# Performance work log

Hardware: AMD Instinct MI355X
Metric: run time of the kernel (lower is better)

## Reference

```python
import jax, jax.numpy as jnp
import numpy as np

B, S, D = 8, 2048, 512

def setup_inputs() -> dict:
    key = jax.random.key(0)
    ks = jax.random.split(key, 9)
    scale = 1.0 / np.sqrt(D)
    return {
        "x": jax.random.normal(ks[0], (B, S, D), dtype=jnp.float32),
        "attention_mask": jax.random.uniform(ks[1], (B, S), dtype=jnp.float32),
        "Wq": jax.random.normal(ks[2], (D, D), dtype=jnp.float32) * scale,
        "bq": jax.random.normal(ks[3], (D,), dtype=jnp.float32) * 0.01,
        "Wk": jax.random.normal(ks[4], (D, D), dtype=jnp.float32) * scale,
        "bk": jax.random.normal(ks[5], (D,), dtype=jnp.float32) * 0.01,
        "Wv": jax.random.normal(ks[6], (D, D), dtype=jnp.float32) * scale,
        "bv": jax.random.normal(ks[7], (D,), dtype=jnp.float32) * 0.01,
    }

def reference(x, attention_mask, Wq, bq, Wk, bk, Wv, bv):
    # Single-head self-attention, full O(S^2) scores as in the original.
    q = jnp.einsum('bsd,df->bsf', x, Wq) + bq  # [B,S,D]
    k = jnp.einsum('bsd,df->bsf', x, Wk) + bk
    v = jnp.einsum('bsd,df->bsf', x, Wv) + bv
    scores = jnp.einsum('bqd,bkd->bqk', q, k) / jnp.sqrt(jnp.float32(D))  # [B,S,S]
    attn = jax.nn.softmax(scores, axis=2)
    weighted = jnp.einsum('bqk,bkd->bqd', attn, v)  # [B,S,D]
    # mask applied multiplicatively to the output, per original code
    return weighted * attention_mask[:, :, None]
```

## Files before the change

### kernel.cpp

```cpp
#include <hip/hip_runtime.h>
#include <math.h>
#include <stdint.h>


typedef _Float16 f16x8 __attribute__((ext_vector_type(8)));
typedef _Float16 f16x4 __attribute__((ext_vector_type(4)));
typedef _Float16 f16x2 __attribute__((ext_vector_type(2)));
typedef float f32x4 __attribute__((ext_vector_type(4)));

__device__ __forceinline__ void async16(const _Float16* g, _Float16* l) {
    __builtin_amdgcn_global_load_lds(
        (const __attribute__((address_space(1))) unsigned int*)(uintptr_t)g,
        (__attribute__((address_space(3))) unsigned int*)(unsigned int)(uintptr_t)l,
        16, 0, 0);
}

__device__ __forceinline__ float frag_sum8(f16x8 v, float acc) {
#if __has_builtin(__builtin_amdgcn_fdot2)
    const f16x2 one2 = {(_Float16)1.f, (_Float16)1.f};
    const f16x2* p = (const f16x2*)&v;
    acc = __builtin_amdgcn_fdot2(p[0], one2, acc, false);
    acc = __builtin_amdgcn_fdot2(p[1], one2, acc, false);
    acc = __builtin_amdgcn_fdot2(p[2], one2, acc, false);
    acc = __builtin_amdgcn_fdot2(p[3], one2, acc, false);
#else
#pragma unroll
    for (int j = 0; j < 8; j++) acc += (float)v[j];
#endif
    return acc;
}

#define MFMA16(a, b, c) __builtin_amdgcn_mfma_f32_16x16x32_f16(a, b, c, 0, 0, 0)
#define BAR() __builtin_amdgcn_s_barrier()
#define LGKM0() asm volatile("s_waitcnt lgkmcnt(0)" ::: "memory")

template <int NT, bool WITH_RS>
__device__ __forceinline__ void core128sq(
    const _Float16* __restrict__ A, const _Float16* __restrict__ B,
    int ld, int row0, int col0, _Float16* sm, f32x4 acc[4][4], float rs[4])
{
    const int tid = threadIdx.x, lane = tid & 63, wave = tid >> 6;
    const int wm = wave >> 1, wn = wave & 1;
    const int rc = lane >> 3;
    const int swz = ((lane & 7) ^ rc) * 8;
    const int fr = lane & 15, q = lane >> 4, fx = fr & 7;
    const size_t laneoff = (size_t)rc * ld + swz;

    const _Float16* gA[4]; int lA[4];
#pragma unroll
    for (int i = 0; i < 4; i++) {
        int c = wave * 4 + i;
        gA[i] = A + (size_t)(row0 + 8 * c) * ld + laneoff;
        lA[i] = c * 512;
    }
    const _Float16* gBe[2]; const _Float16* gBl[2]; int lBe[2], lBl[2];
#pragma unroll
    for (int i = 0; i < 2; i++) {
        int idx = wave * 2 + i;
        int je = (idx & 3) + (idx >> 2) * 8;
        int jl = je + 4;
        gBe[i] = B + (size_t)(col0 + 8 * je) * ld + laneoff;
        gBl[i] = B + (size_t)(col0 + 8 * jl) * ld + laneoff;
        lBe[i] = 8192 + je * 512;
        lBl[i] = 8192 + jl * 512;
    }

#pragma unroll
    for (int i = 0; i < 4; i++) async16(gA[i], sm + lA[i]);
#pragma unroll
    for (int i = 0; i < 2; i++) async16(gBe[i], sm + lBe[i]);
#pragma unroll
    for (int i = 0; i < 2; i++) async16(gBl[i], sm + lBl[i]);
#pragma unroll
    for (int i = 0; i < 4; i++) async16(gA[i] + 64, sm + 16384 + lA[i]);
#pragma unroll
    for (int i = 0; i < 2; i++) async16(gBe[i] + 64, sm + 16384 + lBe[i]);
    asm volatile("s_waitcnt vmcnt(6)" ::: "memory");
    BAR();

#pragma unroll 2
    for (int t = 0; t < NT; ++t) {
        const _Float16* As = sm + (t & 1) * 16384;
        const _Float16* Bs = As + 8192;
        f16x8 af[4][2], b0f[2][2], b1f[2][2];

#pragma unroll
        for (int m = 0; m < 4; m++)
#pragma unroll
            for (int s = 0; s < 2; s++) {
                int ra = wm * 64 + m * 16 + fr;
                af[m][s] = *(const f16x8*)&As[ra * 64 + (((s * 4 + q) ^ fx) * 8)];
            }
#pragma unroll
        for (int n = 0; n < 2; n++)
#pragma unroll
            for (int s = 0; s < 2; s++) {
                int rb = wn * 64 + n * 16 + fr;
                b0f[n][s] = *(const f16x8*)&Bs[rb * 64 + (((s * 4 + q) ^ fx) * 8)];
            }
        if (t + 1 < NT) {
            _Float16* nb = sm + ((t + 1) & 1) * 16384;
#pragma unroll
            for (int i = 0; i < 2; i++)
                async16(gBl[i] + (t + 1) * 64, nb + lBl[i]);
        }
        BAR(); LGKM0();
        if (WITH_RS) {
#pragma unroll
            for (int m = 0; m < 4; m++)
#pragma unroll
                for (int s = 0; s < 2; s++) rs[m] = frag_sum8(af[m][s], rs[m]);
        }
        __builtin_amdgcn_s_setprio(1);
#pragma unroll
        for (int s = 0; s < 2; s++)
#pragma unroll
            for (int m = 0; m < 4; m++)
#pragma unroll
                for (int n = 0; n < 2; n++)
                    acc[m][n] = MFMA16(af[m][s], b0f[n][s], acc[m][n]);
        __builtin_amdgcn_s_setprio(0);
        BAR();

#pragma unroll
        for (int n = 0; n < 2; n++)
#pragma unroll
            for (int s = 0; s < 2; s++) {
                int rb = wn * 64 + (2 + n) * 16 + fr;
                b1f[n][s] = *(const f16x8*)&Bs[rb * 64 + (((s * 4 + q) ^ fx) * 8)];
            }
        if (t + 2 < NT) {
            _Float16* stg = sm + (t & 1) * 16384;
            const int k2 = (t + 2) * 64;
#pragma unroll
            for (int i = 0; i < 4; i++) async16(gA[i] + k2, stg + lA[i]);
#pragma unroll
            for (int i = 0; i < 2; i++) async16(gBe[i] + k2, stg + lBe[i]);
            asm volatile("s_waitcnt vmcnt(6)" ::: "memory");
        } else {
            asm volatile("s_waitcnt vmcnt(0)" ::: "memory");
        }
        BAR(); LGKM0();
        __builtin_amdgcn_s_setprio(1);
#pragma unroll
        for (int s = 0; s < 2; s++)
#pragma unroll
            for (int m = 0; m < 4; m++)
#pragma unroll
                for (int n = 0; n < 2; n++)
                    acc[m][2 + n] = MFMA16(af[m][s], b1f[n][s], acc[m][2 + n]);
        __builtin_amdgcn_s_setprio(0);
        BAR();
    }
}

__global__ __launch_bounds__(256) void prep(
    const float* __restrict__ x,
    const float* __restrict__ Wq, const float* __restrict__ Wk,
    const float* __restrict__ Wv,
    _Float16* __restrict__ Xh,
    _Float16* __restrict__ WqT, _Float16* __restrict__ WkT,
    _Float16* __restrict__ WvT)
{
    const int bid = blockIdx.x;
    if (bid < 8192) {
        int i = (bid * 256 + threadIdx.x) * 4;
        float4 v = *(const float4*)(x + i);
        f16x4 h;
        h.x = (_Float16)v.x; h.y = (_Float16)v.y;
        h.z = (_Float16)v.z; h.w = (_Float16)v.w;
        *(f16x4*)&Xh[i] = h;
    } else {
        int t = bid - 8192;
        int z = t >> 10;
        const float* W = (z == 0) ? Wq : (z == 1) ? Wk : Wv;
        _Float16* Wt   = (z == 0) ? WqT : (z == 1) ? WkT : WvT;
        int idx = (t & 1023) * 256 + threadIdx.x;
        int n = idx >> 9, k = idx & 511;
        Wt[idx] = (_Float16)W[k * 512 + n];
    }
}

__global__ __launch_bounds__(256, 2) void proj_mfma(
    const _Float16* __restrict__ Xh,
    const _Float16* __restrict__ WqT, const float* __restrict__ bq,
    const _Float16* __restrict__ WkT, const float* __restrict__ bk,
    const _Float16* __restrict__ WvT, const float* __restrict__ bv,
    _Float16* __restrict__ Qh, _Float16* __restrict__ Kh,
    _Float16* __restrict__ Vt)
{
    __shared__ __align__(16) _Float16 smem[2 * 16384];
    const int z = blockIdx.z;
    f32x4 acc[4][4];
#pragma unroll
    for (int i = 0; i < 4; i++)
#pragma unroll
        for (int j = 0; j < 4; j++) acc[i][j] = (f32x4){0.f, 0.f, 0.f, 0.f};
    float rs_unused[4];

    const int lane = threadIdx.x & 63, wave = threadIdx.x >> 6;
    const int wm = wave >> 1, wn = wave & 1;
    const int er = (lane >> 4) * 4, ec = lane & 15;

    if (z < 2) {
        const _Float16* Wt = (z == 0) ? WqT : WkT;
        const float* bias  = (z == 0) ? bq : bk;
        _Float16* P        = (z == 0) ? Qh : Kh;
        const float sc     = (z == 0) ? 0.04419417382415922f : 1.0f;
        const int row0 = blockIdx.x * 128, col0 = blockIdx.y * 128;
        core128sq<8, false>(Xh, Wt, 512, row0, col0, smem, acc, rs_unused);
#pragma unroll
        for (int tm = 0; tm < 4; tm++)
#pragma unroll
            for (int tn = 0; tn < 4; tn++) {
                int col = col0 + wn * 64 + tn * 16 + ec;
                float bb = bias[col];
#pragma unroll
                for (int r = 0; r < 4; r++) {
                    int row = row0 + wm * 64 + tm * 16 + er + r;
                    P[(size_t)row * 512 + col] = (_Float16)((acc[tm][tn][r] + bb) * sc);
                }
            }
    } else {
        const int row0 = blockIdx.y * 128;
        const int col0 = blockIdx.x * 128;
        core128sq<8, false>(WvT, Xh, 512, row0, col0, smem, acc, rs_unused);
#pragma unroll
        for (int tm = 0; tm < 4; tm++)
#pragma unroll
            for (int tn = 0; tn < 4; tn++) {
                int col = col0 + wn * 64 + tn * 16 + ec;
                size_t obase = (size_t)(col >> 11) * (512 * 2048) + (col & 2047);
#pragma unroll
                for (int r = 0; r < 4; r++) {
                    int row = row0 + wm * 64 + tm * 16 + er + r;
                    Vt[obase + (size_t)row * 2048] = (_Float16)(acc[tm][tn][r] + bv[row]);
                }
            }
    }
}

__global__ __launch_bounds__(256, 2) void scores_mfma(
    const _Float16* __restrict__ Qh, const _Float16* __restrict__ Kh,
    _Float16* __restrict__ Sh)
{
    __shared__ __align__(16) _Float16 smem[2 * 16384];
    const int bid = blockIdx.x;
    const int b   = bid & 7;
    const int rem = bid >> 3;
    const int col0 = (rem & 15) * 128;
    const int row0 = (rem >> 4) * 128;

    const _Float16* A = Qh + (size_t)b * 2048 * 512;
    const _Float16* B = Kh + (size_t)b * 2048 * 512;
    _Float16* S = Sh + (size_t)b * 2048 * 2048;

    f32x4 acc[4][4];
#pragma unroll
    for (int i = 0; i < 4; i++)
#pragma unroll
        for (int j = 0; j < 4; j++) acc[i][j] = (f32x4){0.f, 0.f, 0.f, 0.f};
    float rs_unused[4];

    core128sq<8, false>(A, B, 512, row0, col0, smem, acc, rs_unused);

    const int lane = threadIdx.x & 63, wave = threadIdx.x >> 6;
    const int wm = wave >> 1, wn = wave & 1;
    const int er = (lane >> 4) * 4, ec = lane & 15;
#pragma unroll
    for (int tm = 0; tm < 4; tm++)
#pragma unroll
        for (int tn = 0; tn < 4; tn++) {
            int col = col0 + wn * 64 + tn * 16 + ec;
#pragma unroll
            for (int r = 0; r < 4; r++) {
                int row = row0 + wm * 64 + tm * 16 + er + r;
                S[(size_t)row * 2048 + col] = (_Float16)__expf(acc[tm][tn][r]);
            }
        }
}

__global__ __launch_bounds__(256, 2) void av_mfma(
    const _Float16* __restrict__ Sh, const _Float16* __restrict__ Vt,
    const float* __restrict__ mask, float* __restrict__ out)
{
    __shared__ __align__(16) _Float16 smem[2 * 16384];
    const int bid = blockIdx.x;
    const int b   = bid & 7;
    const int rem = bid >> 3;
    const int col0 = (rem & 3) * 128;
    const int row0 = (rem >> 2) * 128;

    const _Float16* A = Sh + (size_t)b * 2048 * 2048;
    const _Float16* B = Vt + (size_t)b * 512 * 2048;
    float* O = out + (size_t)b * 2048 * 512;
    const float* mk = mask + (size_t)b * 2048;

    f32x4 acc[4][4];
#pragma unroll
    for (int i = 0; i < 4; i++)
#pragma unroll
        for (int j = 0; j < 4; j++) acc[i][j] = (f32x4){0.f, 0.f, 0.f, 0.f};
    float rs[4] = {0.f, 0.f, 0.f, 0.f};

    core128sq<32, true>(A, B, 2048, row0, col0, smem, acc, rs);

    const int lane = threadIdx.x & 63, wave = threadIdx.x >> 6;
    const int wm = wave >> 1, wn = wave & 1;
    const int er = (lane >> 4) * 4, ec = lane & 15;

#pragma unroll
    for (int tm = 0; tm < 4; tm++) {
        rs[tm] += __shfl_xor(rs[tm], 16, 64);
        rs[tm] += __shfl_xor(rs[tm], 32, 64);
    }
    __syncthreads();
    float* l_s = (float*)smem;
    if (wn == 0 && lane < 16) {
#pragma unroll
        for (int tm = 0; tm < 4; tm++) l_s[wm * 64 + tm * 16 + lane] = rs[tm];
    }
    __syncthreads();

#pragma unroll
    for (int tm = 0; tm < 4; tm++)
#pragma unroll
        for (int r = 0; r < 4; r++) {
            int lrow = wm * 64 + tm * 16 + er + r;
            int row = row0 + lrow;
            float s = mk[row] / l_s[lrow];
#pragma unroll
            for (int tn = 0; tn < 4; tn++) {
                int col = col0 + wn * 64 + tn * 16 + ec;
                O[(size_t)row * 512 + col] = acc[tm][tn][r] * s;
            }
        }
}

extern "C" void kernel_launch(void* const* d_in, const int* in_sizes, int n_in,
                              void* d_out, int out_size, void* d_ws, size_t ws_size,
                              hipStream_t stream) {
    const float* x    = (const float*)d_in[0];
    const float* mask = (const float*)d_in[1];
    const float* Wq   = (const float*)d_in[2];
    const float* bq   = (const float*)d_in[3];
    const float* Wk   = (const float*)d_in[4];
    const float* bk   = (const float*)d_in[5];
    const float* Wv   = (const float*)d_in[6];
    const float* bv   = (const float*)d_in[7];
    float* out = (float*)d_out;

    const size_t BSD = (size_t)8 * 2048 * 512;
    _Float16* base = (_Float16*)d_ws;
    _Float16* Qh  = base;
    _Float16* Kh  = Qh + BSD;
    _Float16* Vt  = Kh + BSD;
    _Float16* WqT = Vt + BSD;
    _Float16* WkT = WqT + 512 * 512;
    _Float16* WvT = WkT + 512 * 512;
    _Float16* Xh  = WvT + 512 * 512;
    _Float16* Sh  = Xh;

    prep<<<dim3(8192 + 3 * 1024), dim3(256), 0, stream>>>(
        x, Wq, Wk, Wv, Xh, WqT, WkT, WvT);
    proj_mfma<<<dim3(128, 4, 3), dim3(256), 0, stream>>>(
        Xh, WqT, bq, WkT, bk, WvT, bv, Qh, Kh, Vt);
    scores_mfma<<<dim3(2048), dim3(256), 0, stream>>>(Qh, Kh, Sh);
    av_mfma<<<dim3(512), dim3(256), 0, stream>>>(Sh, Vt, mask, out);
}
```

Measured before the change: 210.9 us.

## Fuse all four stages into one cooperative persistent kernel with grid syncs

Replaces the four separate launches (prep, projection, scores, AV) with a single cooperative kernel of 512 blocks. It loops over work units per stage and separates stages with grid.sync(). The aim is to remove per-launch overhead and the idle tails between kernels. In exchange, each stage is capped at 512 resident blocks, grid-wide barriers are added, and the old multi-kernel path is kept as a fallback if the cooperative launch fails.

```diff
diff --git a/kernel.cpp b/kernel.cpp
--- a/kernel.cpp
+++ b/kernel.cpp
@@ -1,6 +1,9 @@
 #include <hip/hip_runtime.h>
+#include <hip/hip_cooperative_groups.h>
 #include <math.h>
 #include <stdint.h>
+
+namespace cg = cooperative_groups;
 
 
 typedef _Float16 f16x8 __attribute__((ext_vector_type(8)));
@@ -154,43 +157,39 @@
     }
 }
 
-__global__ __launch_bounds__(256) void prep(
-    const float* __restrict__ x,
+__device__ __forceinline__ void prep_unit(
+    int u, const float* __restrict__ x,
     const float* __restrict__ Wq, const float* __restrict__ Wk,
     const float* __restrict__ Wv,
-    _Float16* __restrict__ Xh,
-    _Float16* __restrict__ WqT, _Float16* __restrict__ WkT,
-    _Float16* __restrict__ WvT)
-{
-    const int bid = blockIdx.x;
-    if (bid < 8192) {
-        int i = (bid * 256 + threadIdx.x) * 4;
+    _Float16* Xh, _Float16* WqT, _Float16* WkT, _Float16* WvT)
+{
+    const int tid = threadIdx.x;
+    if (u < 8192) {
+        int i = (u * 256 + tid) * 4;
         float4 v = *(const float4*)(x + i);
         f16x4 h;
         h.x = (_Float16)v.x; h.y = (_Float16)v.y;
         h.z = (_Float16)v.z; h.w = (_Float16)v.w;
         *(f16x4*)&Xh[i] = h;
     } else {
-        int t = bid - 8192;
+        int t = u - 8192;
         int z = t >> 10;
         const float* W = (z == 0) ? Wq : (z == 1) ? Wk : Wv;
         _Float16* Wt   = (z == 0) ? WqT : (z == 1) ? WkT : WvT;
-        int idx = (t & 1023) * 256 + threadIdx.x;
+        int idx = (t & 1023) * 256 + tid;
         int n = idx >> 9, k = idx & 511;
         Wt[idx] = (_Float16)W[k * 512 + n];
     }
 }
 
-__global__ __launch_bounds__(256, 2) void proj_mfma(
-    const _Float16* __restrict__ Xh,
-    const _Float16* __restrict__ WqT, const float* __restrict__ bq,
-    const _Float16* __restrict__ WkT, const float* __restrict__ bk,
-    const _Float16* __restrict__ WvT, const float* __restrict__ bv,
-    _Float16* __restrict__ Qh, _Float16* __restrict__ Kh,
-    _Float16* __restrict__ Vt)
-{
-    __shared__ __align__(16) _Float16 smem[2 * 16384];
-    const int z = blockIdx.z;
+__device__ __forceinline__ void proj_unit(
+    int u, const _Float16* Xh,
+    const _Float16* WqT, const float* __restrict__ bq,
+    const _Float16* WkT, const float* __restrict__ bk,
+    const _Float16* WvT, const float* __restrict__ bv,
+    _Float16* Qh, _Float16* Kh, _Float16* Vt, _Float16* smem)
+{
+    const int bx = u & 127, by = (u >> 7) & 3, z = u >> 9;
     f32x4 acc[4][4];
 #pragma unroll
     for (int i = 0; i < 4; i++)
@@ -207,7 +206,7 @@
         const float* bias  = (z == 0) ? bq : bk;
         _Float16* P        = (z == 0) ? Qh : Kh;
         const float sc     = (z == 0) ? 0.04419417382415922f : 1.0f;
-        const int row0 = blockIdx.x * 128, col0 = blockIdx.y * 128;
+        const int row0 = bx * 128, col0 = by * 128;
         core128sq<8, false>(Xh, Wt, 512, row0, col0, smem, acc, rs_unused);
 #pragma unroll
         for (int tm = 0; tm < 4; tm++)
@@ -222,8 +221,8 @@
                 }
             }
     } else {
-        const int row0 = blockIdx.y * 128;
-        const int col0 = blockIdx.x * 128;
+        const int row0 = by * 128;
+        const int col0 = bx * 128;
         core128sq<8, false>(WvT, Xh, 512, row0, col0, smem, acc, rs_unused);
 #pragma unroll
         for (int tm = 0; tm < 4; tm++)
@@ -240,14 +239,12 @@
     }
 }
 
-__global__ __launch_bounds__(256, 2) void scores_mfma(
-    const _Float16* __restrict__ Qh, const _Float16* __restrict__ Kh,
-    _Float16* __restrict__ Sh)
-{
-    __shared__ __align__(16) _Float16 smem[2 * 16384];
-    const int bid = blockIdx.x;
-    const int b   = bid & 7;
-    const int rem = bid >> 3;
+__device__ __forceinline__ void scores_unit(
+    int u, const _Float16* Qh, const _Float16* Kh, _Float16* Sh,
+    _Float16* smem)
+{
+    const int b   = u & 7;
+    const int rem = u >> 3;
     const int col0 = (rem & 15) * 128;
     const int row0 = (rem >> 4) * 128;
 
@@ -280,14 +277,12 @@
         }
 }
 
-__global__ __launch_bounds__(256, 2) void av_mfma(
-    const _Float16* __restrict__ Sh, const _Float16* __restrict__ Vt,
-    const float* __restrict__ mask, float* __restrict__ out)
-{
-    __shared__ __align__(16) _Float16 smem[2 * 16384];
-    const int bid = blockIdx.x;
-    const int b   = bid & 7;
-    const int rem = bid >> 3;
+__device__ __forceinline__ void av_unit(
+    int u, const _Float16* Sh, const _Float16* Vt,
+    const float* __restrict__ mask, float* __restrict__ out, _Float16* smem)
+{
+    const int b   = u & 7;
+    const int rem = u >> 3;
     const int col0 = (rem & 3) * 128;
     const int row0 = (rem >> 2) * 128;
 
@@ -335,6 +330,67 @@
                 O[(size_t)row * 512 + col] = acc[tm][tn][r] * s;
             }
         }
+}
+
+__global__ __launch_bounds__(256, 2) void fused_all(
+    const float* __restrict__ x, const float* __restrict__ mask,
+    const float* __restrict__ Wq, const float* __restrict__ bq,
+    const float* __restrict__ Wk, const float* __restrict__ bk,
+    const float* __restrict__ Wv, const float* __restrict__ bv,
+    float* __restrict__ out,
+    _Float16* Qh, _Float16* Kh, _Float16* Vt,
+    _Float16* WqT, _Float16* WkT, _Float16* WvT,
+    _Float16* Xh, _Float16* Sh)
+{
+    __shared__ __align__(16) _Float16 smem[2 * 16384];
+    cg::grid_group grid = cg::this_grid();
+    const int bid = blockIdx.x;
+
+    for (int u = bid; u < 11264; u += 512)
+        prep_unit(u, x, Wq, Wk, Wv, Xh, WqT, WkT, WvT);
+    grid.sync();
+    for (int u = bid; u < 1536; u += 512)
+        proj_unit(u, Xh, WqT, bq, WkT, bk, WvT, bv, Qh, Kh, Vt, smem);
+    grid.sync();
+    for (int u = bid; u < 2048; u += 512)
+        scores_unit(u, Qh, Kh, Sh, smem);
+    grid.sync();
+    av_unit(bid, Sh, Vt, mask, out, smem);
+}
+
+__global__ __launch_bounds__(256) void prep_k(
+    const float* __restrict__ x,
+    const float* __restrict__ Wq, const float* __restrict__ Wk,
+    const float* __restrict__ Wv,
+    _Float16* Xh, _Float16* WqT, _Float16* WkT, _Float16* WvT)
+{
+    prep_unit(blockIdx.x, x, Wq, Wk, Wv, Xh, WqT, WkT, WvT);
+}
+
+__global__ __launch_bounds__(256, 2) void proj_k(
+    const _Float16* Xh,
+    const _Float16* WqT, const float* __restrict__ bq,
+    const _Float16* WkT, const float* __restrict__ bk,
+    const _Float16* WvT, const float* __restrict__ bv,
+    _Float16* Qh, _Float16* Kh, _Float16* Vt)
+{
+    __shared__ __align__(16) _Float16 smem[2 * 16384];
+    proj_unit(blockIdx.x, Xh, WqT, bq, WkT, bk, WvT, bv, Qh, Kh, Vt, smem);
+}
+
+__global__ __launch_bounds__(256, 2) void scores_k(
+    const _Float16* Qh, const _Float16* Kh, _Float16* Sh)
+{
+    __shared__ __align__(16) _Float16 smem[2 * 16384];
+    scores_unit(blockIdx.x, Qh, Kh, Sh, smem);
+}
+
+__global__ __launch_bounds__(256, 2) void av_k(
+    const _Float16* Sh, const _Float16* Vt,
+    const float* __restrict__ mask, float* __restrict__ out)
+{
+    __shared__ __align__(16) _Float16 smem[2 * 16384];
+    av_unit(blockIdx.x, Sh, Vt, mask, out, smem);
 }
 
 extern "C" void kernel_launch(void* const* d_in, const int* in_sizes, int n_in,
@@ -361,10 +417,19 @@
     _Float16* Xh  = WvT + 512 * 512;
     _Float16* Sh  = Xh;
 
-    prep<<<dim3(8192 + 3 * 1024), dim3(256), 0, stream>>>(
-        x, Wq, Wk, Wv, Xh, WqT, WkT, WvT);
-    proj_mfma<<<dim3(128, 4, 3), dim3(256), 0, stream>>>(
-        Xh, WqT, bq, WkT, bk, WvT, bv, Qh, Kh, Vt);
-    scores_mfma<<<dim3(2048), dim3(256), 0, stream>>>(Qh, Kh, Sh);
-    av_mfma<<<dim3(512), dim3(256), 0, stream>>>(Sh, Vt, mask, out);
-}
+    void* kargs[] = {
+        (void*)&x, (void*)&mask, (void*)&Wq, (void*)&bq, (void*)&Wk,
+        (void*)&bk, (void*)&Wv, (void*)&bv, (void*)&out,
+        (void*)&Qh, (void*)&Kh, (void*)&Vt,
+        (void*)&WqT, (void*)&WkT, (void*)&WvT, (void*)&Xh, (void*)&Sh };
+    hipError_t err = hipLaunchCooperativeKernel(
+        (const void*)fused_all, dim3(512), dim3(256), kargs, 0, stream);
+    if (err != hipSuccess) {
+        prep_k<<<dim3(8192 + 3 * 1024), dim3(256), 0, stream>>>(
+            x, Wq, Wk, Wv, Xh, WqT, WkT, WvT);
+        proj_k<<<dim3(1536), dim3(256), 0, stream>>>(
+            Xh, WqT, bq, WkT, bk, WvT, bv, Qh, Kh, Vt);
+        scores_k<<<dim3(2048), dim3(256), 0, stream>>>(Qh, Kh, Sh);
+        av_k<<<dim3(512), dim3(256), 0, stream>>>(Sh, Vt, mask, out);
+    }
+}
```

After: 436.9 us. 107% more time.

## Split each 128x128 MFMA tile across eight waves instead of four

Applied to the files above, without the earlier changes.

The shared GEMM core now runs with 512 threads, so each wave computes a 64x32 sub-tile instead of 64x64. The double-buffered async-to-LDS pipeline is rebuilt so the two A row-halves are staged in separate phases instead of the two B halves, and the av row-sum accumulation is split the same way. All three MFMA kernels use the new core with launch bounds of 512 threads and 4 blocks. The aim is more resident waves per CU to hide load latency, at the cost of more B-fragment LDS reads per FLOP, more barrier traffic, and a tighter per-thread register budget that could cause spills.

```diff
diff --git a/kernel.cpp b/kernel.cpp
--- a/kernel.cpp
+++ b/kernel.cpp
@@ -35,57 +35,45 @@
 #define LGKM0() asm volatile("s_waitcnt lgkmcnt(0)" ::: "memory")
 
 template <int NT, bool WITH_RS>
-__device__ __forceinline__ void core128sq(
+__device__ __forceinline__ void core8w(
     const _Float16* __restrict__ A, const _Float16* __restrict__ B,
-    int ld, int row0, int col0, _Float16* sm, f32x4 acc[4][4], float rs[4])
+    int ld, int row0, int col0, _Float16* sm, f32x4 acc[4][2], float rs[4])
 {
     const int tid = threadIdx.x, lane = tid & 63, wave = tid >> 6;
-    const int wm = wave >> 1, wn = wave & 1;
+    const int wm = wave >> 2, wn = wave & 3;
     const int rc = lane >> 3;
     const int swz = ((lane & 7) ^ rc) * 8;
     const int fr = lane & 15, q = lane >> 4, fx = fr & 7;
     const size_t laneoff = (size_t)rc * ld + swz;
 
-    const _Float16* gA[4]; int lA[4];
-#pragma unroll
-    for (int i = 0; i < 4; i++) {
-        int c = wave * 4 + i;
-        gA[i] = A + (size_t)(row0 + 8 * c) * ld + laneoff;
-        lA[i] = c * 512;
-    }
-    const _Float16* gBe[2]; const _Float16* gBl[2]; int lBe[2], lBl[2];
-#pragma unroll
-    for (int i = 0; i < 2; i++) {
-        int idx = wave * 2 + i;
-        int je = (idx & 3) + (idx >> 2) * 8;
-        int jl = je + 4;
-        gBe[i] = B + (size_t)(col0 + 8 * je) * ld + laneoff;
-        gBl[i] = B + (size_t)(col0 + 8 * jl) * ld + laneoff;
-        lBe[i] = 8192 + je * 512;
-        lBl[i] = 8192 + jl * 512;
-    }
-
-#pragma unroll
-    for (int i = 0; i < 4; i++) async16(gA[i], sm + lA[i]);
-#pragma unroll
-    for (int i = 0; i < 2; i++) async16(gBe[i], sm + lBe[i]);
-#pragma unroll
-    for (int i = 0; i < 2; i++) async16(gBl[i], sm + lBl[i]);
-#pragma unroll
-    for (int i = 0; i < 4; i++) async16(gA[i] + 64, sm + 16384 + lA[i]);
-#pragma unroll
-    for (int i = 0; i < 2; i++) async16(gBe[i] + 64, sm + 16384 + lBe[i]);
-    asm volatile("s_waitcnt vmcnt(6)" ::: "memory");
+    const int ah0c = (wave & 3) + (wave >> 2) * 8;
+    const int ah1c = ah0c + 4;
+    const int b0c = 2 * wave, b1c = b0c + 1;
+    const _Float16* gAh0 = A + (size_t)(row0 + 8 * ah0c) * ld + laneoff;
+    const _Float16* gAh1 = A + (size_t)(row0 + 8 * ah1c) * ld + laneoff;
+    const _Float16* gB0  = B + (size_t)(col0 + 8 * b0c) * ld + laneoff;
+    const _Float16* gB1  = B + (size_t)(col0 + 8 * b1c) * ld + laneoff;
+    const int lAh0 = ah0c * 512, lAh1 = ah1c * 512;
+    const int lB0 = 8192 + b0c * 512, lB1 = 8192 + b1c * 512;
+
+    async16(gAh0, sm + lAh0);
+    async16(gAh1, sm + lAh1);
+    async16(gB0,  sm + lB0);
+    async16(gB1,  sm + lB1);
+    async16(gB0 + 64,  sm + 16384 + lB0);
+    async16(gB1 + 64,  sm + 16384 + lB1);
+    async16(gAh0 + 64, sm + 16384 + lAh0);
+    asm volatile("s_waitcnt vmcnt(3)" ::: "memory");
     BAR();
 
 #pragma unroll 2
     for (int t = 0; t < NT; ++t) {
         const _Float16* As = sm + (t & 1) * 16384;
         const _Float16* Bs = As + 8192;
-        f16x8 af[4][2], b0f[2][2], b1f[2][2];
-
-#pragma unroll
-        for (int m = 0; m < 4; m++)
+        f16x8 af[2][2], bf[2][2];
+
+#pragma unroll
+        for (int m = 0; m < 2; m++)
 #pragma unroll
             for (int s = 0; s < 2; s++) {
                 int ra = wm * 64 + m * 16 + fr;
@@ -95,19 +83,15 @@
         for (int n = 0; n < 2; n++)
 #pragma unroll
             for (int s = 0; s < 2; s++) {
-                int rb = wn * 64 + n * 16 + fr;
-                b0f[n][s] = *(const f16x8*)&Bs[rb * 64 + (((s * 4 + q) ^ fx) * 8)];
-            }
-        if (t + 1 < NT) {
-            _Float16* nb = sm + ((t + 1) & 1) * 16384;
-#pragma unroll
-            for (int i = 0; i < 2; i++)
-                async16(gBl[i] + (t + 1) * 64, nb + lBl[i]);
-        }
+                int rb = wn * 32 + n * 16 + fr;
+                bf[n][s] = *(const f16x8*)&Bs[rb * 64 + (((s * 4 + q) ^ fx) * 8)];
+            }
+        if (t + 1 < NT)
+            async16(gAh1 + (t + 1) * 64, sm + ((t + 1) & 1) * 16384 + lAh1);
         BAR(); LGKM0();
         if (WITH_RS) {
 #pragma unroll
-            for (int m = 0; m < 4; m++)
+            for (int m = 0; m < 2; m++)
 #pragma unroll
                 for (int s = 0; s < 2; s++) rs[m] = frag_sum8(af[m][s], rs[m]);
         }
@@ -115,41 +99,48 @@
 #pragma unroll
         for (int s = 0; s < 2; s++)
 #pragma unroll
-            for (int m = 0; m < 4; m++)
+            for (int m = 0; m < 2; m++)
 #pragma unroll
                 for (int n = 0; n < 2; n++)
-                    acc[m][n] = MFMA16(af[m][s], b0f[n][s], acc[m][n]);
+                    acc[m][n] = MFMA16(af[m][s], bf[n][s], acc[m][n]);
         __builtin_amdgcn_s_setprio(0);
         BAR();
 
 #pragma unroll
-        for (int n = 0; n < 2; n++)
+        for (int m = 0; m < 2; m++)
 #pragma unroll
             for (int s = 0; s < 2; s++) {
-                int rb = wn * 64 + (2 + n) * 16 + fr;
-                b1f[n][s] = *(const f16x8*)&Bs[rb * 64 + (((s * 4 + q) ^ fx) * 8)];
+                int ra = wm * 64 + (2 + m) * 16 + fr;
+                af[m][s] = *(const f16x8*)&As[ra * 64 + (((s * 4 + q) ^ fx) * 8)];
             }
         if (t + 2 < NT) {
             _Float16* stg = sm + (t & 1) * 16384;
             const int k2 = (t + 2) * 64;
-#pragma unroll
-            for (int i = 0; i < 4; i++) async16(gA[i] + k2, stg + lA[i]);
-#pragma unroll
-            for (int i = 0; i < 2; i++) async16(gBe[i] + k2, stg + lBe[i]);
-            asm volatile("s_waitcnt vmcnt(6)" ::: "memory");
+            async16(gB0 + k2,  stg + lB0);
+            async16(gB1 + k2,  stg + lB1);
+            async16(gAh0 + k2, stg + lAh0);
+        }
+        BAR(); LGKM0();
+        if (WITH_RS) {
+#pragma unroll
+            for (int m = 0; m < 2; m++)
+#pragma unroll
+                for (int s = 0; s < 2; s++) rs[2 + m] = frag_sum8(af[m][s], rs[2 + m]);
+        }
+        __builtin_amdgcn_s_setprio(1);
+#pragma unroll
+        for (int s = 0; s < 2; s++)
+#pragma unroll
+            for (int m = 0; m < 2; m++)
+#pragma unroll
+                for (int n = 0; n < 2; n++)
+                    acc[2 + m][n] = MFMA16(af[m][s], bf[n][s], acc[2 + m][n]);
+        __builtin_amdgcn_s_setprio(0);
+        if (t + 2 < NT) {
+            asm volatile("s_waitcnt vmcnt(3)" ::: "memory");
         } else {
             asm volatile("s_waitcnt vmcnt(0)" ::: "memory");
         }
-        BAR(); LGKM0();
-        __builtin_amdgcn_s_setprio(1);
-#pragma unroll
-        for (int s = 0; s < 2; s++)
-#pragma unroll
-            for (int m = 0; m < 4; m++)
-#pragma unroll
-                for (int n = 0; n < 2; n++)
-                    acc[m][2 + n] = MFMA16(af[m][s], b1f[n][s], acc[m][2 + n]);
-        __builtin_amdgcn_s_setprio(0);
         BAR();
     }
 }
@@ -181,7 +172,7 @@
     }
 }
 
-__global__ __launch_bounds__(256, 2) void proj_mfma(
+__global__ __launch_bounds__(512, 4) void proj_mfma(
     const _Float16* __restrict__ Xh,
     const _Float16* __restrict__ WqT, const float* __restrict__ bq,
     const _Float16* __restrict__ WkT, const float* __restrict__ bk,
@@ -191,15 +182,15 @@
 {
     __shared__ __align__(16) _Float16 smem[2 * 16384];
     const int z = blockIdx.z;
-    f32x4 acc[4][4];
+    f32x4 acc[4][2];
 #pragma unroll
     for (int i = 0; i < 4; i++)
 #pragma unroll
-        for (int j = 0; j < 4; j++) acc[i][j] = (f32x4){0.f, 0.f, 0.f, 0.f};
+        for (int j = 0; j < 2; j++) acc[i][j] = (f32x4){0.f, 0.f, 0.f, 0.f};
     float rs_unused[4];
 
     const int lane = threadIdx.x & 63, wave = threadIdx.x >> 6;
-    const int wm = wave >> 1, wn = wave & 1;
+    const int wm = wave >> 2, wn = wave & 3;
     const int er = (lane >> 4) * 4, ec = lane & 15;
 
     if (z < 2) {
@@ -208,12 +199,12 @@
         _Float16* P        = (z == 0) ? Qh : Kh;
         const float sc     = (z == 0) ? 0.04419417382415922f : 1.0f;
         const int row0 = blockIdx.x * 128, col0 = blockIdx.y * 128;
-        core128sq<8, false>(Xh, Wt, 512, row0, col0, smem, acc, rs_unused);
+        core8w<8, false>(Xh, Wt, 512, row0, col0, smem, acc, rs_unused);
 #pragma unroll
         for (int tm = 0; tm < 4; tm++)
 #pragma unroll
-            for (int tn = 0; tn < 4; tn++) {
-                int col = col0 + wn * 64 + tn * 16 + ec;
+            for (int tn = 0; tn < 2; tn++) {
+                int col = col0 + wn * 32 + tn * 16 + ec;
                 float bb = bias[col];
 #pragma unroll
                 for (int r = 0; r < 4; r++) {
@@ -224,12 +215,12 @@
     } else {
         const int row0 = blockIdx.y * 128;
         const int col0 = blockIdx.x * 128;
-        core128sq<8, false>(WvT, Xh, 512, row0, col0, smem, acc, rs_unused);
+        core8w<8, false>(WvT, Xh, 512, row0, col0, smem, acc, rs_unused);
 #pragma unroll
         for (int tm = 0; tm < 4; tm++)
 #pragma unroll
-            for (int tn = 0; tn < 4; tn++) {
-                int col = col0 + wn * 64 + tn * 16 + ec;
+            for (int tn = 0; tn < 2; tn++) {
+                int col = col0 + wn * 32 + tn * 16 + ec;
                 size_t obase = (size_t)(col >> 11) * (512 * 2048) + (col & 2047);
 #pragma unroll
                 for (int r = 0; r < 4; r++) {
@@ -240,7 +231,7 @@
     }
 }
 
-__global__ __launch_bounds__(256, 2) void scores_mfma(
+__global__ __launch_bounds__(512, 4) void scores_mfma(
     const _Float16* __restrict__ Qh, const _Float16* __restrict__ Kh,
     _Float16* __restrict__ Sh)
 {
@@ -255,23 +246,23 @@
     const _Float16* B = Kh + (size_t)b * 2048 * 512;
     _Float16* S = Sh + (size_t)b * 2048 * 2048;
 
-    f32x4 acc[4][4];
+    f32x4 acc[4][2];
 #pragma unroll
     for (int i = 0; i < 4; i++)
 #pragma unroll
-        for (int j = 0; j < 4; j++) acc[i][j] = (f32x4){0.f, 0.f, 0.f, 0.f};
+        for (int j = 0; j < 2; j++) acc[i][j] = (f32x4){0.f, 0.f, 0.f, 0.f};
     float rs_unused[4];
 
-    core128sq<8, false>(A, B, 512, row0, col0, smem, acc, rs_unused);
+    core8w<8, false>(A, B, 512, row0, col0, smem, acc, rs_unused);
 
     const int lane = threadIdx.x & 63, wave = threadIdx.x >> 6;
-    const int wm = wave >> 1, wn = wave & 1;
+    const int wm = wave >> 2, wn = wave & 3;
     const int er = (lane >> 4) * 4, ec = lane & 15;
 #pragma unroll
     for (int tm = 0; tm < 4; tm++)
 #pragma unroll
-        for (int tn = 0; tn < 4; tn++) {
-            int col = col0 + wn * 64 + tn * 16 + ec;
+        for (int tn = 0; tn < 2; tn++) {
+            int col = col0 + wn * 32 + tn * 16 + ec;
 #pragma unroll
             for (int r = 0; r < 4; r++) {
                 int row = row0 + wm * 64 + tm * 16 + er + r;
@@ -280,7 +271,7 @@
         }
 }
 
-__global__ __launch_bounds__(256, 2) void av_mfma(
+__global__ __launch_bounds__(512, 4) void av_mfma(
     const _Float16* __restrict__ Sh, const _Float16* __restrict__ Vt,
     const float* __restrict__ mask, float* __restrict__ out)
 {
@@ -296,17 +287,17 @@
     float* O = out + (size_t)b * 2048 * 512;
     const float* mk = mask + (size_t)b * 2048;
 
-    f32x4 acc[4][4];
+    f32x4 acc[4][2];
 #pragma unroll
     for (int i = 0; i < 4; i++)
 #pragma unroll
-        for (int j = 0; j < 4; j++) acc[i][j] = (f32x4){0.f, 0.f, 0.f, 0.f};
+        for (int j = 0; j < 2; j++) acc[i][j] = (f32x4){0.f, 0.f, 0.f, 0.f};
     float rs[4] = {0.f, 0.f, 0.f, 0.f};
 
-    core128sq<32, true>(A, B, 2048, row0, col0, smem, acc, rs);
+    core8w<32, true>(A, B, 2048, row0, col0, smem, acc, rs);
 
     const int lane = threadIdx.x & 63, wave = threadIdx.x >> 6;
-    const int wm = wave >> 1, wn = wave & 1;
+    const int wm = wave >> 2, wn = wave & 3;
     const int er = (lane >> 4) * 4, ec = lane & 15;
 
 #pragma unroll
@@ -330,8 +321,8 @@
             int row = row0 + lrow;
             float s = mk[row] / l_s[lrow];
 #pragma unroll
-            for (int tn = 0; tn < 4; tn++) {
-                int col = col0 + wn * 64 + tn * 16 + ec;
+            for (int tn = 0; tn < 2; tn++) {
+                int col = col0 + wn * 32 + tn * 16 + ec;
                 O[(size_t)row * 512 + col] = acc[tm][tn][r] * s;
             }
         }
@@ -363,8 +354,8 @@
 
     prep<<<dim3(8192 + 3 * 1024), dim3(256), 0, stream>>>(
         x, Wq, Wk, Wv, Xh, WqT, WkT, WvT);
-    proj_mfma<<<dim3(128, 4, 3), dim3(256), 0, stream>>>(
+    proj_mfma<<<dim3(128, 4, 3), dim3(512), 0, stream>>>(
         Xh, WqT, bq, WkT, bk, WvT, bv, Qh, Kh, Vt);
-    scores_mfma<<<dim3(2048), dim3(256), 0, stream>>>(Qh, Kh, Sh);
-    av_mfma<<<dim3(512), dim3(256), 0, stream>>>(Sh, Vt, mask, out);
-}
+    scores_mfma<<<dim3(2048), dim3(512), 0, stream>>>(Qh, Kh, Sh);
+    av_mfma<<<dim3(512), dim3(512), 0, stream>>>(Sh, Vt, mask, out);
+}
```

Result: slower. 246.2 us (+16.7%).
